# Optimization experiments

Measured on AMD Instinct MI355X. Metric: run time of the kernel, lower is better.

## Reference

```python
import jax, jax.numpy as jnp
import numpy as np

FEATS_HOP = 441
FFT_LENS = (1024, 2048, 4096)
LOG_EPS = 1e-16
NUM_MEL = 80


def _frame(wp, f):
    """Strided framing with the original's front-zero-padding of short tail frames.
    wp: [B, Tp] -> [B, n, f], n = ceil(Tp / FEATS_HOP)."""
    B, Tp = wp.shape
    n = -(-Tp // FEATS_HOP)
    starts = jnp.arange(n) * FEATS_HOP                      # [n]
    pad = jnp.maximum(starts + f - Tp, 0)                   # zeros prepended per short frame
    j = jnp.arange(f)                                       # [f]
    idx = jnp.clip(starts[:, None] + j[None, :] - pad[:, None], 0, Tp - 1)  # [n, f]
    mask = (j[None, :] >= pad[:, None]).astype(wp.dtype)    # [n, f]
    return wp[:, idx] * mask[None]                          # [B, n, f]


def _log_mel(x, window, mel, f):
    # pad f//2 zeros at the start of time (as in the torch code)
    wp = jnp.pad(x, ((0, 0), (f // 2, 0)))
    fr = _frame(wp, f) * window                             # [B, n, f]
    h = f // 2
    fr = jnp.concatenate([fr[..., h:], fr[..., :h]], axis=-1)  # half swap
    spec = jnp.fft.rfft(fr)                                 # [B, n, f//2+1]
    pow_spec = spec.real ** 2 + spec.imag ** 2
    return jnp.log(pow_spec @ mel + LOG_EPS)                # [B, n, 80]


def setup_inputs() -> dict:
    key = jax.random.key(0)
    ks = jax.random.split(key, 7)
    B, T = 8, 882000
    inp = {"x": jax.random.normal(ks[0], (B, T), dtype=jnp.float32)}
    for i, f in enumerate(FFT_LENS):
        inp["window_{}".format(f)] = jax.random.uniform(ks[1 + 2 * i], (f,), dtype=jnp.float32)
        inp["mel_{}".format(f)] = jax.random.uniform(ks[2 + 2 * i], (f // 2 + 1, NUM_MEL), dtype=jnp.float32)
    return inp


def reference(x, window_1024, mel_1024, window_2048, mel_2048, window_4096, mel_4096):
    windows = {1024: window_1024, 2048: window_2048, 4096: window_4096}
    mels = {1024: mel_1024, 2048: mel_2048, 4096: mel_4096}
    feats = []
    n0 = None
    for f in FFT_LENS:
        lm = _log_mel(x, windows[f], mels[f], f)            # [B, n_f, 80]
        if n0 is None:
            n0 = lm.shape[1]
        feats.append(lm[:, :n0])
    return jnp.stack(feats, axis=-1)                        # [B, n0, 80, 3]
```

## Files before the change

kernel.cpp:

```cpp
#include <hip/hip_runtime.h>
#include <math.h>

#define HOP 441
#define NMEL 80

typedef __attribute__((ext_vector_type(8))) short bf16x8;
typedef __attribute__((ext_vector_type(4))) float f32x4;

__device__ __forceinline__ float2 cmulf(float2 a, float2 b) {
    return make_float2(a.x * b.x - a.y * b.y, a.x * b.y + a.y * b.x);
}
__device__ __forceinline__ float2 cadd(float2 a, float2 b) {
    return make_float2(a.x + b.x, a.y + b.y);
}
__device__ __forceinline__ float2 csub(float2 a, float2 b) {
    return make_float2(a.x - b.x, a.y - b.y);
}
__device__ __forceinline__ float2 shx2(float2 v, int m) {
    return make_float2(__shfl_xor(v.x, m, 64), __shfl_xor(v.y, m, 64));
}
__device__ __forceinline__ float2 shidx2(float2 v, int src) {
    return make_float2(__shfl(v.x, src, 64), __shfl(v.y, src, 64));
}
__device__ __forceinline__ int brev6f(int v) {
    return ((v & 1) << 5) | ((v & 2) << 3) | ((v & 4) << 1) |
           ((v & 8) >> 1) | ((v & 16) >> 3) | ((v & 32) >> 5);
}
__device__ __forceinline__ int brevn(int v, int bits) {
    int r = 0;
    for (int i = 0; i < bits; ++i) r |= ((v >> i) & 1) << (bits - 1 - i);
    return r;
}
__device__ __forceinline__ float2 w32t(int m) {
    constexpr float C[16] = {1.0f, 0.980785280f, 0.923879533f, 0.831469612f,
                             0.707106781f, 0.555570233f, 0.382683432f, 0.195090322f,
                             0.0f, -0.195090322f, -0.382683432f, -0.555570233f,
                             -0.707106781f, -0.831469612f, -0.923879533f, -0.980785280f};
    constexpr float S[16] = {0.0f, 0.195090322f, 0.382683432f, 0.555570233f,
                             0.707106781f, 0.831469612f, 0.923879533f, 0.980785280f,
                             1.0f, 0.980785280f, 0.923879533f, 0.831469612f,
                             0.707106781f, 0.555570233f, 0.382683432f, 0.195090322f};
    return make_float2(C[m], -S[m]);
}
__device__ __forceinline__ unsigned short bf16t(float v) {
    return (unsigned short)(__float_as_uint(v) >> 16);
}

template<int FLEN, int KPAD>
__device__ __forceinline__ void fft_body(const float* __restrict__ x, const float* __restrict__ win,
                                         unsigned short* __restrict__ pows_g, int T, int n0,
                                         int bx, int b, uint4* __restrict__ powsU) {
    constexpr int N    = FLEN / 2;
    constexpr int R    = N / 64;
    constexpr int LOGR = (R == 32) ? 5 : ((R == 16) ? 4 : 3);
    constexpr int R2_  = R / 2;
    constexpr int HALF = FLEN / 2;
    constexpr int NOCT = KPAD / 8;
    constexpr float PI = 3.14159265358979f;

    unsigned short* ldsw = (unsigned short*)powsU + (threadIdx.x >> 6) * KPAD;

    const int tid = threadIdx.x;
    const int sub = tid >> 6;
    const int p   = tid & 63;
    const int s   = brev6f(p);
    const int t0  = bx * 4;

    if (p < KPAD - (N + 1)) ldsw[N + 1 + p] = 0;

    float2 W32s, W16s, W8s, W4s, W2s, wl, Pp, ub;
    float sg32, sg16, sg8, sg4, sg2, sg1;
    {
        float s_, c_;
        __sincosf(-PI * (float)(p & 31) / 32.0f, &s_, &c_);
        W32s = (p & 32) ? make_float2(c_, s_) : make_float2(1.0f, 0.0f);
        sg32 = (p & 32) ? -1.0f : 1.0f;
        __sincosf(-PI * (float)(p & 15) / 16.0f, &s_, &c_);
        W16s = (p & 16) ? make_float2(c_, s_) : make_float2(1.0f, 0.0f);
        sg16 = (p & 16) ? -1.0f : 1.0f;
        __sincosf(-PI * (float)(p & 7) / 8.0f, &s_, &c_);
        W8s  = (p & 8) ? make_float2(c_, s_) : make_float2(1.0f, 0.0f);
        sg8  = (p & 8) ? -1.0f : 1.0f;
        __sincosf(-PI * (float)(p & 3) / 4.0f, &s_, &c_);
        W4s  = (p & 4) ? make_float2(c_, s_) : make_float2(1.0f, 0.0f);
        sg4  = (p & 4) ? -1.0f : 1.0f;
        __sincosf(-PI * (float)(p & 1) / 2.0f, &s_, &c_);
        W2s  = (p & 2) ? make_float2(c_, s_) : make_float2(1.0f, 0.0f);
        sg2  = (p & 2) ? -1.0f : 1.0f;
        sg1  = (p & 1) ? -1.0f : 1.0f;
        __sincosf(-2.0f * PI * (float)p / (float)N, &s_, &c_); wl = make_float2(c_, s_);
        __sincosf(PI * (float)s / 64.0f, &s_, &c_);             Pp = make_float2(c_, s_);
        __sincosf(PI / (float)N, &s_, &c_);                     ub = make_float2(c_, s_);
    }
    const int mpart = brev6f((64 - s) & 63);

    const float* xb = x + (size_t)b * (size_t)T;
    const int Tp = T + HALF;

    const int t = t0 + sub;
    const bool valid = (t < n0);
    const int start = HOP * t;
    int pad = start + FLEN - Tp; if (pad < 0) pad = 0;
    const int base = start - pad - HALF;

    float2 z[R];
    if (pad == 0 && base >= 0 && valid) {
        const float*  xp = xb + base + 2 * p;
        const float2* wp = ((const float2*)win) + p;
        #pragma unroll
        for (int j = 0; j < R; ++j) {
            const int q = brevn(j, LOGR);
            const float2 wv = wp[64 * q];
            z[j] = make_float2(xp[128 * q] * wv.x, xp[128 * q + 1] * wv.y);
        }
    } else {
        #pragma unroll
        for (int j = 0; j < R; ++j) {
            const int q  = brevn(j, LOGR);
            const int i  = 64 * q + p;
            const int j0 = 2 * i;
            const float2 wv = ((const float2*)win)[i];
            const int xi0 = base + j0;
            float v0 = (valid && j0 >= pad     && xi0 >= 0)     ? xb[xi0] * wv.x     : 0.0f;
            float v1 = (valid && j0 + 1 >= pad && xi0 + 1 >= 0) ? xb[xi0 + 1] * wv.y : 0.0f;
            z[j] = make_float2(v0, v1);
        }
    }

    #pragma unroll
    for (int h = 1; h < R; h <<= 1) {
        #pragma unroll
        for (int base2 = 0; base2 < R; base2 += 2 * h) {
            #pragma unroll
            for (int i = 0; i < h; ++i) {
                const float2 W  = w32t((16 * i) / h);
                const float2 tt = cmulf(W, z[base2 + i + h]);
                const float2 aa = z[base2 + i];
                z[base2 + i]     = cadd(aa, tt);
                z[base2 + i + h] = csub(aa, tt);
            }
        }
    }

    {
        const float2 w2c = cmulf(wl, wl);
        const float2 w3c = cmulf(w2c, wl);
        const float2 w4c = cmulf(w2c, w2c);
        z[1] = cmulf(z[1], wl);
        z[2] = cmulf(z[2], w2c);
        z[3] = cmulf(z[3], w3c);
        float2 a0 = w4c, a1 = cmulf(wl, w4c), a2 = cmulf(w2c, w4c), a3 = cmulf(w3c, w4c);
        #pragma unroll
        for (int g = 4; g < R; g += 4) {
            z[g]     = cmulf(z[g],     a0);
            z[g + 1] = cmulf(z[g + 1], a1);
            z[g + 2] = cmulf(z[g + 2], a2);
            z[g + 3] = cmulf(z[g + 3], a3);
            if (g + 4 < R) {
                a0 = cmulf(a0, w4c); a1 = cmulf(a1, w4c);
                a2 = cmulf(a2, w4c); a3 = cmulf(a3, w4c);
            }
        }
    }

#define XSTAGE(MASK, W, SG) { \
        _Pragma("unroll") \
        for (int j = 0; j < R; ++j) { \
            const float2 xq = shx2(z[j], MASK); \
            const float2 d  = make_float2(fmaf(SG, z[j].x, xq.x), \
                                          fmaf(SG, z[j].y, xq.y)); \
            z[j] = cmulf(d, W); \
        } }
    XSTAGE(32, W32s, sg32)
    XSTAGE(16, W16s, sg16)
    XSTAGE(8,  W8s,  sg8)
    XSTAGE(4,  W4s,  sg4)
    XSTAGE(2,  W2s,  sg2)
    #pragma unroll
    for (int j = 0; j < R; ++j) {
        const float2 xq = shx2(z[j], 1);
        z[j] = make_float2(fmaf(sg1, z[j].x, xq.x), fmaf(sg1, z[j].y, xq.y));
    }
#undef XSTAGE

#define SWZK(KK) (((KK) & ~(R - 1)) | (((KK) & (R - 1)) ^ (((KK) >> LOGR) & (R - 1))))
#define PAIRE(RR, ZK, ZN, CW, SW) { \
        const float Er = (ZK).x + (ZN).x, Ei = (ZK).y - (ZN).y; \
        const float Or = (ZK).y + (ZN).y, Oi = -((ZK).x - (ZN).x); \
        const float Tr = (CW) * Or + (SW) * Oi; \
        const float Ti = (CW) * Oi - (SW) * Or; \
        const float Xr0 = Er + Tr, Xi0 = Ei + Ti; \
        const float Xr1 = Er - Tr, Xi1 = Ei - Ti; \
        const float pw0 = 0.25f * (Xr0 * Xr0 + Xi0 * Xi0); \
        const float pw1 = 0.25f * (Xr1 * Xr1 + Xi1 * Xi1); \
        const int k0b = R * s + (RR); \
        const int km  = N - k0b; \
        ldsw[SWZK(k0b)] = bf16t(pw0); \
        ldsw[SWZK(km)]  = bf16t(pw1); }

    {
        const float2 ub2 = cmulf(ub, ub);
        const float2 ub4 = cmulf(ub2, ub2);
        float2 c0 = Pp, c1 = cmulf(Pp, ub), c2 = cmulf(Pp, ub2), c3 = cmulf(c1, ub2);
        {
            const float2 Zn = shidx2(z[0], mpart);
            PAIRE(0, z[0], Zn, c0.x, c0.y)
        }
        { const float2 Zn = shx2(z[R - 1], 63); PAIRE(1, z[1], Zn, c1.x, c1.y) }
        { const float2 Zn = shx2(z[R - 2], 63); PAIRE(2, z[2], Zn, c2.x, c2.y) }
        { const float2 Zn = shx2(z[R - 3], 63); PAIRE(3, z[3], Zn, c3.x, c3.y) }
        #pragma unroll
        for (int g = 4; g <= R2_; g += 4) {
            c0 = cmulf(c0, ub4); c1 = cmulf(c1, ub4);
            c2 = cmulf(c2, ub4); c3 = cmulf(c3, ub4);
            { const float2 Zn = shx2(z[R - g], 63); PAIRE(g, z[g], Zn, c0.x, c0.y) }
            if (g + 1 <= R2_) { const float2 Zn = shx2(z[R - g - 1], 63); PAIRE(g + 1, z[g + 1], Zn, c1.x, c1.y) }
            if (g + 2 <= R2_) { const float2 Zn = shx2(z[R - g - 2], 63); PAIRE(g + 2, z[g + 2], Zn, c2.x, c2.y) }
            if (g + 3 <= R2_) { const float2 Zn = shx2(z[R - g - 3], 63); PAIRE(g + 3, z[g + 3], Zn, c3.x, c3.y) }
        }
    }
#undef PAIRE
#undef SWZK

    if (valid) {
        const uint4* src = powsU + sub * (KPAD / 8);
        uint4* dst = (uint4*)(pows_g + (size_t)((size_t)b * n0 + t) * KPAD);
        #pragma unroll
        for (int w = 0; w < (NOCT + 63) / 64; ++w) {
            const int oct = p + 64 * w;
            if (oct < NOCT) dst[oct] = src[oct];
        }
    }
}

template<int KPAD, int LOGR, int R, int K>
__device__ __forceinline__ void melcvt_one(const float* __restrict__ mel,
                                           unsigned short* __restrict__ melT, int idx) {
    const int n = idx / KPAD, pos = idx - n * KPAD;
    const int k = (pos & ~(R - 1)) | ((pos & (R - 1)) ^ ((pos >> LOGR) & (R - 1)));
    unsigned short v = 0;
    if (k < K) {
        const unsigned u = __float_as_uint(mel[(size_t)k * NMEL + n]);
        v = (unsigned short)((u + 0x7FFF + ((u >> 16) & 1)) >> 16);
    }
    melT[(size_t)n * KPAD + pos] = v;
}

template<int KPAD, int SZI>
__device__ __forceinline__ void gemm_body(const unsigned short* __restrict__ powsA,
                                          const unsigned short* __restrict__ melT,
                                          float* __restrict__ out, int Mvalid, int gbid) {
    constexpr int NCH = KPAD / 32;

    const int tid = threadIdx.x;
    const int w   = tid >> 6;
    const int l   = tid & 63;
    const int frame0 = gbid * 64 + w * 16;

    const unsigned short* Ap = powsA + (size_t)(frame0 + (l & 15)) * KPAD + (l >> 4) * 8;
    const unsigned short* Bp = melT + (size_t)(l & 15) * KPAD + (l >> 4) * 8;

    f32x4 acc[5];
    const f32x4 z4 = {0.0f, 0.0f, 0.0f, 0.0f};
    #pragma unroll
    for (int nt = 0; nt < 5; ++nt) acc[nt] = z4;

    #pragma unroll 2
    for (int c = 0; c < NCH; ++c) {
        const bf16x8 a = *(const bf16x8*)(Ap + c * 32);
        #pragma unroll
        for (int nt = 0; nt < 5; ++nt) {
            const bf16x8 bb = *(const bf16x8*)(Bp + (size_t)nt * 16 * KPAD + c * 32);
            acc[nt] = __builtin_amdgcn_mfma_f32_16x16x32_bf16(a, bb, acc[nt], 0, 0, 0);
        }
    }

    #pragma unroll
    for (int nt = 0; nt < 5; ++nt) {
        #pragma unroll
        for (int q = 0; q < 4; ++q) {
            const int row = (l >> 4) * 4 + q;
            const int col = nt * 16 + (l & 15);
            const int frame = frame0 + row;
            if (frame < Mvalid)
                out[((size_t)frame * NMEL + col) * 3 + SZI] = logf(acc[nt][q] + 1e-16f);
        }
    }
}

__global__ __launch_bounds__(256, 4)
void k_ffts(const float* __restrict__ x,
            const float* __restrict__ w1, const float* __restrict__ w2, const float* __restrict__ w4,
            const float* __restrict__ m1, const float* __restrict__ m2, const float* __restrict__ m4,
            unsigned short* __restrict__ p1, unsigned short* __restrict__ p2, unsigned short* __restrict__ p4,
            unsigned short* __restrict__ m1t, unsigned short* __restrict__ m2t, unsigned short* __restrict__ m4t,
            int T, int n0, int gx) {
    __shared__ uint4 sh[4 * 2080 / 8];
    int bid = blockIdx.x;
    const int nf = gx * 8;
    if (bid < nf) { fft_body<4096, 2080>(x, w4, p4, T, n0, bid % gx, bid / gx, sh); return; }
    bid -= nf;
    if (bid < nf) { fft_body<2048, 1056>(x, w2, p2, T, n0, bid % gx, bid / gx, sh); return; }
    bid -= nf;
    if (bid < nf) { fft_body<1024,  544>(x, w1, p1, T, n0, bid % gx, bid / gx, sh); return; }
    bid -= nf;
    int idx = bid * 256 + (int)threadIdx.x;
    constexpr int S1 = NMEL * 544, S2 = NMEL * 1056, S4 = NMEL * 2080;
    if (idx < S1) { melcvt_one< 544, 3,  8,  513>(m1, m1t, idx); return; }
    idx -= S1;
    if (idx < S2) { melcvt_one<1056, 4, 16, 1025>(m2, m2t, idx); return; }
    idx -= S2;
    if (idx < S4) melcvt_one<2080, 5, 32, 2049>(m4, m4t, idx);
}

__global__ __launch_bounds__(256)
void k_gemms(const unsigned short* __restrict__ p1, const unsigned short* __restrict__ p2,
             const unsigned short* __restrict__ p4,
             const unsigned short* __restrict__ m1t, const unsigned short* __restrict__ m2t,
             const unsigned short* __restrict__ m4t,
             float* __restrict__ out, int Mvalid, int ngemm) {
    int bid = blockIdx.x;
    if (bid < ngemm) { gemm_body<2080, 2>(p4, m4t, out, Mvalid, bid); return; }
    bid -= ngemm;
    if (bid < ngemm) { gemm_body<1056, 1>(p2, m2t, out, Mvalid, bid); return; }
    bid -= ngemm;
    gemm_body< 544, 0>(p1, m1t, out, Mvalid, bid);
}

template<int FLEN, int SZI>
__global__ __launch_bounds__(512, 4)
void spect_kernel(const float* __restrict__ x, const float* __restrict__ win,
                  const float* __restrict__ mel, float* __restrict__ out,
                  int T, int n0) {
    constexpr int N    = FLEN / 2;
    constexpr int R    = N / 64;
    constexpr int LOGR = (R == 32) ? 5 : ((R == 16) ? 4 : 3);
    constexpr int R2_  = R / 2;
    constexpr int K    = N + 1;
    constexpr int KP   = N + 8;
    constexpr int HALF = FLEN / 2;
    constexpr int NT   = 512;
    constexpr int FPB  = 8;
    constexpr float PI = 3.14159265358979f;

    __shared__ uint4 pows4[KP];
    __shared__ float res[FPB * NMEL];
    unsigned short* pows = (unsigned short*)pows4;

    const int tid = threadIdx.x;
    const int sub = tid >> 6;
    const int p   = tid & 63;
    const int s   = brev6f(p);
    const int b   = blockIdx.y;
    const int t0  = blockIdx.x * FPB;

    for (int i = tid; i < FPB * NMEL; i += NT) res[i] = 0.0f;

    float2 W32s, W16s, W8s, W4s, W2s, wl, Pp, ub;
    float sg32, sg16, sg8, sg4, sg2, sg1;
    {
        float s_, c_;
        __sincosf(-PI * (float)(p & 31) / 32.0f, &s_, &c_);
        W32s = (p & 32) ? make_float2(c_, s_) : make_float2(1.0f, 0.0f);
        sg32 = (p & 32) ? -1.0f : 1.0f;
        __sincosf(-PI * (float)(p & 15) / 16.0f, &s_, &c_);
        W16s = (p & 16) ? make_float2(c_, s_) : make_float2(1.0f, 0.0f);
        sg16 = (p & 16) ? -1.0f : 1.0f;
        __sincosf(-PI * (float)(p & 7) / 8.0f, &s_, &c_);
        W8s  = (p & 8) ? make_float2(c_, s_) : make_float2(1.0f, 0.0f);
        sg8  = (p & 8) ? -1.0f : 1.0f;
        __sincosf(-PI * (float)(p & 3) / 4.0f, &s_, &c_);
        W4s  = (p & 4) ? make_float2(c_, s_) : make_float2(1.0f, 0.0f);
        sg4  = (p & 4) ? -1.0f : 1.0f;
        __sincosf(-PI * (float)(p & 1) / 2.0f, &s_, &c_);
        W2s  = (p & 2) ? make_float2(c_, s_) : make_float2(1.0f, 0.0f);
        sg2  = (p & 2) ? -1.0f : 1.0f;
        sg1  = (p & 1) ? -1.0f : 1.0f;
        __sincosf(-2.0f * PI * (float)p / (float)N, &s_, &c_); wl = make_float2(c_, s_);
        __sincosf(PI * (float)s / 64.0f, &s_, &c_);             Pp = make_float2(c_, s_);
        __sincosf(PI / (float)N, &s_, &c_);                     ub = make_float2(c_, s_);
    }
    const int mpart = brev6f((64 - s) & 63);

    const float* xb = x + (size_t)b * (size_t)T;
    const int Tp = T + HALF;

    const int t = t0 + sub;
    const bool valid = (t < n0);
    const int start = HOP * t;
    int pad = start + FLEN - Tp; if (pad < 0) pad = 0;
    const int base = start - pad - HALF;

    float2 z[R];
    if (pad == 0 && base >= 0 && valid) {
        const float*  xp = xb + base + 2 * p;
        const float2* wp = ((const float2*)win) + p;
        #pragma unroll
        for (int j = 0; j < R; ++j) {
            const int q = brevn(j, LOGR);
            const float2 wv = wp[64 * q];
            z[j] = make_float2(xp[128 * q] * wv.x, xp[128 * q + 1] * wv.y);
        }
    } else {
        #pragma unroll
        for (int j = 0; j < R; ++j) {
            const int q  = brevn(j, LOGR);
            const int i  = 64 * q + p;
            const int j0 = 2 * i;
            const float2 wv = ((const float2*)win)[i];
            const int xi0 = base + j0;
            float v0 = (valid && j0 >= pad     && xi0 >= 0)     ? xb[xi0] * wv.x     : 0.0f;
            float v1 = (valid && j0 + 1 >= pad && xi0 + 1 >= 0) ? xb[xi0 + 1] * wv.y : 0.0f;
            z[j] = make_float2(v0, v1);
        }
    }

    #pragma unroll
    for (int h = 1; h < R; h <<= 1) {
        #pragma unroll
        for (int base2 = 0; base2 < R; base2 += 2 * h) {
            #pragma unroll
            for (int i = 0; i < h; ++i) {
                const float2 W  = w32t((16 * i) / h);
                const float2 tt = cmulf(W, z[base2 + i + h]);
                const float2 aa = z[base2 + i];
                z[base2 + i]     = cadd(aa, tt);
                z[base2 + i + h] = csub(aa, tt);
            }
        }
    }

    {
        const float2 w2c = cmulf(wl, wl);
        const float2 w3c = cmulf(w2c, wl);
        const float2 w4c = cmulf(w2c, w2c);
        z[1] = cmulf(z[1], wl);
        z[2] = cmulf(z[2], w2c);
        z[3] = cmulf(z[3], w3c);
        float2 a0 = w4c, a1 = cmulf(wl, w4c), a2 = cmulf(w2c, w4c), a3 = cmulf(w3c, w4c);
        #pragma unroll
        for (int g = 4; g < R; g += 4) {
            z[g]     = cmulf(z[g],     a0);
            z[g + 1] = cmulf(z[g + 1], a1);
            z[g + 2] = cmulf(z[g + 2], a2);
            z[g + 3] = cmulf(z[g + 3], a3);
            if (g + 4 < R) {
                a0 = cmulf(a0, w4c); a1 = cmulf(a1, w4c);
                a2 = cmulf(a2, w4c); a3 = cmulf(a3, w4c);
            }
        }
    }

#define XSTAGE(MASK, W, SG) { \
        _Pragma("unroll") \
        for (int j = 0; j < R; ++j) { \
            const float2 xq = shx2(z[j], MASK); \
            const float2 d  = make_float2(fmaf(SG, z[j].x, xq.x), \
                                          fmaf(SG, z[j].y, xq.y)); \
            z[j] = cmulf(d, W); \
        } }
    XSTAGE(32, W32s, sg32)
    XSTAGE(16, W16s, sg16)
    XSTAGE(8,  W8s,  sg8)
    XSTAGE(4,  W4s,  sg4)
    XSTAGE(2,  W2s,  sg2)
    #pragma unroll
    for (int j = 0; j < R; ++j) {
        const float2 xq = shx2(z[j], 1);
        z[j] = make_float2(fmaf(sg1, z[j].x, xq.x), fmaf(sg1, z[j].y, xq.y));
    }
#undef XSTAGE

#define PAIRE(RR, ZK, ZN, CW, SW) { \
        const float Er = 0.5f * ((ZK).x + (ZN).x), Ei = 0.5f * ((ZK).y - (ZN).y); \
        const float Or = 0.5f * ((ZK).y + (ZN).y), Oi = -0.5f * ((ZK).x - (ZN).x); \
        const float Tr = (CW) * Or + (SW) * Oi; \
        const float Ti = (CW) * Oi - (SW) * Or; \
        const float Xr0 = Er + Tr, Xi0 = Ei + Ti; \
        const float Xr1 = Er - Tr, Xi1 = Ei - Ti; \
        const float pw0 = Xr0 * Xr0 + Xi0 * Xi0; \
        const float pw1 = Xr1 * Xr1 + Xi1 * Xi1; \
        const int k0b  = R * s + (RR); \
        const int km   = N - k0b; \
        const int row0 = (k0b & ~(R - 1)) | ((k0b & (R - 1)) ^ (s & 7)); \
        const int row1 = (km  & ~(R - 1)) | ((km  & (R - 1)) ^ ((km >> LOGR) & 7)); \
        pows[row0 * 8 + sub] = bf16t(pw0); \
        pows[row1 * 8 + sub] = bf16t(pw1); }

    {
        const float2 ub2 = cmulf(ub, ub);
        const float2 ub4 = cmulf(ub2, ub2);
        float2 c0 = Pp, c1 = cmulf(Pp, ub), c2 = cmulf(Pp, ub2), c3 = cmulf(c1, ub2);
        {
            const float2 Zn = shidx2(z[0], mpart);
            PAIRE(0, z[0], Zn, c0.x, c0.y)
        }
        { const float2 Zn = shx2(z[R - 1], 63); PAIRE(1, z[1], Zn, c1.x, c1.y) }
        { const float2 Zn = shx2(z[R - 2], 63); PAIRE(2, z[2], Zn, c2.x, c2.y) }
        { const float2 Zn = shx2(z[R - 3], 63); PAIRE(3, z[3], Zn, c3.x, c3.y) }
        #pragma unroll
        for (int g = 4; g <= R2_; g += 4) {
            c0 = cmulf(c0, ub4); c1 = cmulf(c1, ub4);
            c2 = cmulf(c2, ub4); c3 = cmulf(c3, ub4);
            { const float2 Zn = shx2(z[R - g], 63); PAIRE(g, z[g], Zn, c0.x, c0.y) }
            if (g + 1 <= R2_) { const float2 Zn = shx2(z[R - g - 1], 63); PAIRE(g + 1, z[g + 1], Zn, c1.x, c1.y) }
            if (g + 2 <= R2_) { const float2 Zn = shx2(z[R - g - 2], 63); PAIRE(g + 2, z[g + 2], Zn, c2.x, c2.y) }
            if (g + 3 <= R2_) { const float2 Zn = shx2(z[R - g - 3], 63); PAIRE(g + 3, z[g + 3], Zn, c3.x, c3.y) }
        }
    }
#undef PAIRE

    __syncthreads();

    constexpr int NCH = 25;
    constexpr int CH  = (K + NCH - 1) / NCH;
    if (tid < NCH * 20) {
        const int g  = tid % 20;
        const int cc = tid / 20;
        const int k0 = cc * CH;
        const int k1 = (k0 + CH < K) ? (k0 + CH) : K;
        float acc[FPB][4];
        #pragma unroll
        for (int f2 = 0; f2 < FPB; ++f2) {
            acc[f2][0] = 0.f; acc[f2][1] = 0.f; acc[f2][2] = 0.f; acc[f2][3] = 0.f;
        }
        #pragma unroll 4
        for (int k = k0; k < k1; ++k) {
            const int kmel = (k & ~(R - 1)) | ((k & (R - 1)) ^ ((k >> LOGR) & 7));
            const float4 mr = *(const float4*)(mel + (size_t)kmel * NMEL + 4 * g);
            const uint4 pv = pows4[k];
#define ACC2(W32, BASE) { \
            const float p0 = __uint_as_float((W32) << 16); \
            const float p1 = __uint_as_float((W32) & 0xFFFF0000u); \
            acc[BASE][0] += p0 * mr.x; acc[BASE][1] += p0 * mr.y; \
            acc[BASE][2] += p0 * mr.z; acc[BASE][3] += p0 * mr.w; \
            acc[(BASE)+1][0] += p1 * mr.x; acc[(BASE)+1][1] += p1 * mr.y; \
            acc[(BASE)+1][2] += p1 * mr.z; acc[(BASE)+1][3] += p1 * mr.w; }
            ACC2(pv.x, 0) ACC2(pv.y, 2) ACC2(pv.z, 4) ACC2(pv.w, 6)
#undef ACC2
        }
        #pragma unroll
        for (int f2 = 0; f2 < FPB; ++f2) {
            #pragma unroll
            for (int mi = 0; mi < 4; ++mi) {
                atomicAdd(&res[f2 * NMEL + 4 * g + mi], acc[f2][mi]);
            }
        }
    }
    __syncthreads();

    const size_t outbase = (size_t)b * (size_t)n0 * NMEL * 3;
    for (int i = tid; i < FPB * NMEL; i += NT) {
        const int f2 = i / NMEL;
        const int m  = i % NMEL;
        const int tt = t0 + f2;
        if (tt < n0) {
            out[outbase + ((size_t)tt * NMEL + m) * 3 + SZI] = logf(res[i] + 1e-16f);
        }
    }
}

extern "C" void kernel_launch(void* const* d_in, const int* in_sizes, int n_in,
                              void* d_out, int out_size, void* d_ws, size_t ws_size,
                              hipStream_t stream) {
    const float* x  = (const float*)d_in[0];
    const float* w1 = (const float*)d_in[1];
    const float* m1 = (const float*)d_in[2];
    const float* w2 = (const float*)d_in[3];
    const float* m2 = (const float*)d_in[4];
    const float* w4 = (const float*)d_in[5];
    const float* m4 = (const float*)d_in[6];
    float* out = (float*)d_out;

    const int B  = 8;
    const int T  = in_sizes[0] / B;
    const int n0 = (T + 512 + 440) / 441;

    const size_t M    = (size_t)B * (size_t)n0;
    const size_t Mpad = (M + 63) & ~(size_t)63;
    const size_t KP1 = 544, KP2 = 1056, KP4 = 2080;
    const size_t need = (Mpad + NMEL) * (KP1 + KP2 + KP4) * 2;

    if (ws_size >= need) {
        unsigned short* p1  = (unsigned short*)d_ws;
        unsigned short* p2  = p1 + Mpad * KP1;
        unsigned short* p4  = p2 + Mpad * KP2;
        unsigned short* m1t = p4 + Mpad * KP4;
        unsigned short* m2t = m1t + NMEL * KP1;
        unsigned short* m4t = m2t + NMEL * KP2;

        const int gx  = (n0 + 3) / 4;
        const int nf  = gx * 8;
        const int cvt = (NMEL * (544 + 1056 + 2080) + 255) / 256;
        const int ngemm = (int)(Mpad / 64);

        k_ffts<<<3 * nf + cvt, 256, 0, stream>>>(x, w1, w2, w4, m1, m2, m4,
                                                 p1, p2, p4, m1t, m2t, m4t, T, n0, gx);
        k_gemms<<<3 * ngemm, 256, 0, stream>>>(p1, p2, p4, m1t, m2t, m4t,
                                               out, (int)M, ngemm);
    } else {
        const int gxf = (n0 + 7) / 8;
        spect_kernel<1024, 0><<<dim3(gxf, B), 512, 0, stream>>>(x, w1, m1, out, T, n0);
        spect_kernel<2048, 1><<<dim3(gxf, B), 512, 0, stream>>>(x, w2, m2, out, T, n0);
        spect_kernel<4096, 2><<<dim3(gxf, B), 512, 0, stream>>>(x, w4, m4, out, T, n0);
    }
}
```

Measured before the change: 202.2 us.

## Split mel GEMM blocks across the five 16-column output tiles

Each GEMM block now computes a single 16-column mel tile for a 64-frame tile instead of all five, and the grid grows fivefold. The aim is more blocks and waves in flight, fewer accumulator registers and higher occupancy for the latency-bound MFMA loop. The cost is that each A-row chunk (the power spectra) is loaded five times by different blocks instead of once, which raises global and L2 traffic.

```diff
diff --git a/kernel.cpp b/kernel.cpp
--- a/kernel.cpp
+++ b/kernel.cpp
@@ -249,42 +249,34 @@
 template<int KPAD, int SZI>
 __device__ __forceinline__ void gemm_body(const unsigned short* __restrict__ powsA,
                                           const unsigned short* __restrict__ melT,
-                                          float* __restrict__ out, int Mvalid, int gbid) {
+                                          float* __restrict__ out, int Mvalid,
+                                          int ftile, int nt) {
     constexpr int NCH = KPAD / 32;
 
     const int tid = threadIdx.x;
     const int w   = tid >> 6;
     const int l   = tid & 63;
-    const int frame0 = gbid * 64 + w * 16;
+    const int frame0 = ftile * 64 + w * 16;
 
     const unsigned short* Ap = powsA + (size_t)(frame0 + (l & 15)) * KPAD + (l >> 4) * 8;
-    const unsigned short* Bp = melT + (size_t)(l & 15) * KPAD + (l >> 4) * 8;
-
-    f32x4 acc[5];
-    const f32x4 z4 = {0.0f, 0.0f, 0.0f, 0.0f};
+    const unsigned short* Bp = melT + (size_t)(nt * 16 + (l & 15)) * KPAD + (l >> 4) * 8;
+
+    f32x4 acc = {0.0f, 0.0f, 0.0f, 0.0f};
+
+    #pragma unroll 4
+    for (int c = 0; c < NCH; ++c) {
+        const bf16x8 a  = *(const bf16x8*)(Ap + c * 32);
+        const bf16x8 bb = *(const bf16x8*)(Bp + c * 32);
+        acc = __builtin_amdgcn_mfma_f32_16x16x32_bf16(a, bb, acc, 0, 0, 0);
+    }
+
     #pragma unroll
-    for (int nt = 0; nt < 5; ++nt) acc[nt] = z4;
-
-    #pragma unroll 2
-    for (int c = 0; c < NCH; ++c) {
-        const bf16x8 a = *(const bf16x8*)(Ap + c * 32);
-        #pragma unroll
-        for (int nt = 0; nt < 5; ++nt) {
-            const bf16x8 bb = *(const bf16x8*)(Bp + (size_t)nt * 16 * KPAD + c * 32);
-            acc[nt] = __builtin_amdgcn_mfma_f32_16x16x32_bf16(a, bb, acc[nt], 0, 0, 0);
-        }
-    }
-
-    #pragma unroll
-    for (int nt = 0; nt < 5; ++nt) {
-        #pragma unroll
-        for (int q = 0; q < 4; ++q) {
-            const int row = (l >> 4) * 4 + q;
-            const int col = nt * 16 + (l & 15);
-            const int frame = frame0 + row;
-            if (frame < Mvalid)
-                out[((size_t)frame * NMEL + col) * 3 + SZI] = logf(acc[nt][q] + 1e-16f);
-        }
+    for (int q = 0; q < 4; ++q) {
+        const int row = (l >> 4) * 4 + q;
+        const int col = nt * 16 + (l & 15);
+        const int frame = frame0 + row;
+        if (frame < Mvalid)
+            out[((size_t)frame * NMEL + col) * 3 + SZI] = logf(acc[q] + 1e-16f);
     }
 }
 
@@ -320,11 +312,12 @@
              const unsigned short* __restrict__ m4t,
              float* __restrict__ out, int Mvalid, int ngemm) {
     int bid = blockIdx.x;
-    if (bid < ngemm) { gemm_body<2080, 2>(p4, m4t, out, Mvalid, bid); return; }
-    bid -= ngemm;
-    if (bid < ngemm) { gemm_body<1056, 1>(p2, m2t, out, Mvalid, bid); return; }
-    bid -= ngemm;
-    gemm_body< 544, 0>(p1, m1t, out, Mvalid, bid);
+    const int n5 = ngemm * 5;
+    if (bid < n5) { gemm_body<2080, 2>(p4, m4t, out, Mvalid, bid / 5, bid % 5); return; }
+    bid -= n5;
+    if (bid < n5) { gemm_body<1056, 1>(p2, m2t, out, Mvalid, bid / 5, bid % 5); return; }
+    bid -= n5;
+    gemm_body< 544, 0>(p1, m1t, out, Mvalid, bid / 5, bid % 5);
 }
 
 template<int FLEN, int SZI>
@@ -596,8 +589,8 @@
 
         k_ffts<<<3 * nf + cvt, 256, 0, stream>>>(x, w1, w2, w4, m1, m2, m4,
                                                  p1, p2, p4, m1t, m2t, m4t, T, n0, gx);
-        k_gemms<<<3 * ngemm, 256, 0, stream>>>(p1, p2, p4, m1t, m2t, m4t,
-                                               out, (int)M, ngemm);
+        k_gemms<<<15 * ngemm, 256, 0, stream>>>(p1, p2, p4, m1t, m2t, m4t,
+                                                out, (int)M, ngemm);
     } else {
         const int gxf = (n0 + 7) / 8;
         spect_kernel<1024, 0><<<dim3(gxf, B), 512, 0, stream>>>(x, w1, m1, out, T, n0);
```

Result: slower. 242.6 us (+20.0%).

## Split GEMM K-dimension across warps with shared-memory reduction

Applied to the files above, without the earlier changes.

The mel GEMM previously gave each of the four waves its own 16-frame tile. Now each block handles a single 16-frame tile, and the four waves split the K (frequency) chunks between them. Partial accumulators are reduced through shared memory before the log and store. This launches four times as many blocks to improve parallelism and latency hiding, at the cost of a block-level sync, shared-memory traffic, and the first wave doing all the output work.

```diff
diff --git a/kernel.cpp b/kernel.cpp
--- a/kernel.cpp
+++ b/kernel.cpp
@@ -249,15 +249,15 @@
 template<int KPAD, int SZI>
 __device__ __forceinline__ void gemm_body(const unsigned short* __restrict__ powsA,
                                           const unsigned short* __restrict__ melT,
-                                          float* __restrict__ out, int Mvalid, int gbid) {
+                                          float* __restrict__ out, int Mvalid, int mt,
+                                          float* __restrict__ red) {
     constexpr int NCH = KPAD / 32;
 
     const int tid = threadIdx.x;
     const int w   = tid >> 6;
     const int l   = tid & 63;
-    const int frame0 = gbid * 64 + w * 16;
-
-    const unsigned short* Ap = powsA + (size_t)(frame0 + (l & 15)) * KPAD + (l >> 4) * 8;
+
+    const unsigned short* Ap = powsA + (size_t)(mt * 16 + (l & 15)) * KPAD + (l >> 4) * 8;
     const unsigned short* Bp = melT + (size_t)(l & 15) * KPAD + (l >> 4) * 8;
 
     f32x4 acc[5];
@@ -265,8 +265,10 @@
     #pragma unroll
     for (int nt = 0; nt < 5; ++nt) acc[nt] = z4;
 
-    #pragma unroll 2
-    for (int c = 0; c < NCH; ++c) {
+    const int cpw = (NCH + 3) >> 2;
+    const int c0 = w * cpw;
+    const int c1 = (c0 + cpw < NCH) ? (c0 + cpw) : NCH;
+    for (int c = c0; c < c1; ++c) {
         const bf16x8 a = *(const bf16x8*)(Ap + c * 32);
         #pragma unroll
         for (int nt = 0; nt < 5; ++nt) {
@@ -275,15 +277,32 @@
         }
     }
 
-    #pragma unroll
-    for (int nt = 0; nt < 5; ++nt) {
-        #pragma unroll
-        for (int q = 0; q < 4; ++q) {
-            const int row = (l >> 4) * 4 + q;
-            const int col = nt * 16 + (l & 15);
-            const int frame = frame0 + row;
-            if (frame < Mvalid)
-                out[((size_t)frame * NMEL + col) * 3 + SZI] = logf(acc[nt][q] + 1e-16f);
+    if (w > 0) {
+        #pragma unroll
+        for (int nt = 0; nt < 5; ++nt) {
+            #pragma unroll
+            for (int q = 0; q < 4; ++q) {
+                const int row = (l >> 4) * 4 + q;
+                const int col = nt * 16 + (l & 15);
+                red[(w - 1) * 16 * NMEL + row * NMEL + col] = acc[nt][q];
+            }
+        }
+    }
+    __syncthreads();
+    if (w == 0) {
+        #pragma unroll
+        for (int nt = 0; nt < 5; ++nt) {
+            #pragma unroll
+            for (int q = 0; q < 4; ++q) {
+                const int row = (l >> 4) * 4 + q;
+                const int col = nt * 16 + (l & 15);
+                float v = acc[nt][q] + red[0 * 16 * NMEL + row * NMEL + col]
+                        + red[1 * 16 * NMEL + row * NMEL + col]
+                        + red[2 * 16 * NMEL + row * NMEL + col];
+                const int frame = mt * 16 + row;
+                if (frame < Mvalid)
+                    out[((size_t)frame * NMEL + col) * 3 + SZI] = logf(v + 1e-16f);
+            }
         }
     }
 }
@@ -318,13 +337,14 @@
              const unsigned short* __restrict__ p4,
              const unsigned short* __restrict__ m1t, const unsigned short* __restrict__ m2t,
              const unsigned short* __restrict__ m4t,
-             float* __restrict__ out, int Mvalid, int ngemm) {
+             float* __restrict__ out, int Mvalid, int ntile) {
+    __shared__ float red[3 * 16 * NMEL];
     int bid = blockIdx.x;
-    if (bid < ngemm) { gemm_body<2080, 2>(p4, m4t, out, Mvalid, bid); return; }
-    bid -= ngemm;
-    if (bid < ngemm) { gemm_body<1056, 1>(p2, m2t, out, Mvalid, bid); return; }
-    bid -= ngemm;
-    gemm_body< 544, 0>(p1, m1t, out, Mvalid, bid);
+    if (bid < ntile) { gemm_body<2080, 2>(p4, m4t, out, Mvalid, bid, red); return; }
+    bid -= ntile;
+    if (bid < ntile) { gemm_body<1056, 1>(p2, m2t, out, Mvalid, bid, red); return; }
+    bid -= ntile;
+    gemm_body< 544, 0>(p1, m1t, out, Mvalid, bid, red);
 }
 
 template<int FLEN, int SZI>
@@ -592,12 +612,12 @@
         const int gx  = (n0 + 3) / 4;
         const int nf  = gx * 8;
         const int cvt = (NMEL * (544 + 1056 + 2080) + 255) / 256;
-        const int ngemm = (int)(Mpad / 64);
+        const int ntile = (int)(Mpad / 16);
 
         k_ffts<<<3 * nf + cvt, 256, 0, stream>>>(x, w1, w2, w4, m1, m2, m4,
                                                  p1, p2, p4, m1t, m2t, m4t, T, n0, gx);
-        k_gemms<<<3 * ngemm, 256, 0, stream>>>(p1, p2, p4, m1t, m2t, m4t,
-                                               out, (int)M, ngemm);
+        k_gemms<<<3 * ntile, 256, 0, stream>>>(p1, p2, p4, m1t, m2t, m4t,
+                                               out, (int)M, ntile);
     } else {
         const int gxf = (n0 + 7) / 8;
         spect_kernel<1024, 0><<<dim3(gxf, B), 512, 0, stream>>>(x, w1, m1, out, T, n0);
```

After: 209.9 us. +3.8%, slower.
